# Performance work log

Measured on AMD Instinct MI355X. Metric: run time of the kernel, lower is better.

## Reference

```python
import jax, jax.numpy as jnp
import numpy as np

BETA = 0.25


def setup_inputs() -> dict:
    key = jax.random.key(0)
    k1, k2 = jax.random.split(key)
    x = jax.random.normal(k1, (32, 64, 64, 64), dtype=jnp.float32)   # [B, C, H, W]
    emb = jax.random.normal(k2, (1024, 64), dtype=jnp.float32)       # [K, C] codebook
    return {"x": x, "emb": emb}


def reference(x, emb):
    b, c, h, w = x.shape
    # (b h w) c
    z = jnp.transpose(x, (0, 2, 3, 1)).reshape(-1, c)
    # squared euclidean distances (argmin identical to torch.cdist argmin)
    # ||z||^2 - 2 z e^T + ||e||^2, never taking sqrt since only argmin is used
    d = (jnp.sum(z * z, axis=1, keepdims=True)
         - 2.0 * jnp.einsum('nc,kc->nk', z, emb)
         + jnp.sum(emb * emb, axis=1)[None, :])        # [N, K]
    idx = jnp.argmin(d, axis=1)                        # [N] int
    e = emb[idx]                                       # gather [N, C]
    e = jnp.transpose(e.reshape(b, h, w, c), (0, 3, 1, 2))  # [B, C, H, W]
    codebook_loss = jnp.mean((jax.lax.stop_gradient(x) - e) ** 2)
    commitment_loss = BETA * jnp.mean((x - jax.lax.stop_gradient(e)) ** 2)
    loss = codebook_loss + commitment_loss
    o = x + jax.lax.stop_gradient(e - x)               # straight-through
    indices = idx.reshape(b, h, w)
    return (o, loss, indices)
```

## Files before the change

kernel.cpp:

```cpp
#include <hip/hip_runtime.h>

#define BATCH   32
#define CCH     64
#define HW      4096
#define NPIX    (BATCH * HW)
#define KCODES  1024
#define NELEM   (NPIX * CCH)
#define MB      256
#define CK      64
#define MARGIN_Q 3u

typedef _Float16 f16;
typedef __attribute__((ext_vector_type(8))) _Float16 f16x8;
typedef __attribute__((ext_vector_type(4))) float    f32x4;

static __device__ __forceinline__ f32x4 mfma16(f16x8 a, f16x8 b, f32x4 c) {
    return __builtin_amdgcn_mfma_f32_16x16x32_f16(a, b, c, 0, 0, 0);
}

static __device__ __forceinline__ void dma16(void* lds, const void* g) {
    __builtin_amdgcn_global_load_lds(
        (const __attribute__((address_space(1))) unsigned int*)g,
        (__attribute__((address_space(3))) unsigned int*)lds, 16, 0, 0);
}

#define WS_EEB_F   64
#define WS_CBH_B   8192
#define WS_CBL_B   139264
#define WS_WL_U    67584

__global__ __launch_bounds__(256) void vq_prep(
    const float* __restrict__ emb, float* __restrict__ wsf,
    unsigned* __restrict__ wsu, f16* __restrict__ cbH, f16* __restrict__ cbL,
    float* __restrict__ eeb_g)
{
    const int t = threadIdx.x;
    if (blockIdx.x < 32) {
        const int gid = blockIdx.x * 256 + t;
        const int row = gid >> 3, gi = gid & 7;
        const float* src = emb + (size_t)row * CCH + gi * 8;
        float4 v0 = *(const float4*)(src);
        float4 v1 = *(const float4*)(src + 4);
        float vv[8] = {v0.x, v0.y, v0.z, v0.w, v1.x, v1.y, v1.z, v1.w};
        f16x8 h, l;
#pragma unroll
        for (int j = 0; j < 8; ++j) {
            f16 hh = (f16)vv[j];
            h[j] = hh;
            l[j] = (f16)(vv[j] - (float)hh);
        }
        const int off = row * 64 + 8 * (gi ^ (row & 7));
        *(f16x8*)(cbH + off) = h;
        *(f16x8*)(cbL + off) = l;
    } else {
        if (t == 0) { wsf[0] = 0.f; wsu[1] = 0u; }
        for (int r = t * 4; r < t * 4 + 4; ++r) {
            const float4* row4 = (const float4*)(emb + (size_t)r * CCH);
            float s = 0.f;
#pragma unroll
            for (int i = 0; i < 16; ++i) {
                float4 v = row4[i];
                s = fmaf(v.x, v.x, s); s = fmaf(v.y, v.y, s);
                s = fmaf(v.z, v.z, s); s = fmaf(v.w, v.w, s);
            }
            eeb_g[r] = fmaf(s, 2048.0f, 1048576.0f);
        }
    }
}

__global__ __launch_bounds__(256, 2) void vq_main(
    const float* __restrict__ x,
    const float* __restrict__ emb,
    const f16* __restrict__ cbH, const f16* __restrict__ cbL,
    const float* __restrict__ eeb_g,
    float* __restrict__ o, float* __restrict__ idx_out,
    float* __restrict__ acc, unsigned* __restrict__ wl_count,
    unsigned* __restrict__ wl, unsigned cap)
{
    __shared__ __align__(16) char smem[32768];
    __shared__ float eebl[2][CK];
    __shared__ unsigned bu1[MB], bu2[MB];
    __shared__ float wred[4];

    const int t    = threadIdx.x;
    const int lane = t & 63;
    const int w    = t >> 6;
    const int col  = lane & 15;
    const int quad = lane >> 4;
    const int c7   = col & 7;
    const int sw0  = 8 * (quad ^ c7);
    const int sw1  = sw0 ^ 32;
    const int n0   = blockIdx.x * MB;
    const int b    = n0 >> 12;
    const int p0   = n0 & 4095;
    const float* xb = x + (size_t)b * (CCH * HW) + p0;

    auto stage = [&](int chunk, int bufi) {
        const int k0 = chunk * CK;
        char* lb = smem + bufi * 16384;
        const char* gH = (const char*)cbH + (size_t)k0 * 128 + w * 2048 + lane * 16;
        const char* gL = (const char*)cbL + (size_t)k0 * 128 + w * 2048 + lane * 16;
        char* lH = lb + w * 2048;
        char* lL = lb + 8192 + w * 2048;
        dma16(lH,        gH);
        dma16(lH + 1024, gH + 1024);
        dma16(lL,        gL);
        dma16(lL + 1024, gL + 1024);
        if (t < CK) eebl[bufi][t] = eeb_g[k0 + t];
    };

    stage(0, 0);

    f16x8 aH[4][2], aL[4][2];
#pragma unroll
    for (int rt = 0; rt < 4; ++rt) {
        const int pp = w * 64 + rt * 16 + col;
#pragma unroll
        for (int kc = 0; kc < 2; ++kc) {
            f16x8 h, l;
#pragma unroll
            for (int j = 0; j < 8; ++j) {
                const int c = kc * 32 + quad * 8 + j;
                float zs = -2.0f * xb[(size_t)c * HW + pp];
                f16 hh = (f16)zs;
                h[j] = hh;
                l[j] = (f16)(zs - (float)hh);
            }
            aH[rt][kc] = h;
            aL[rt][kc] = l;
        }
    }

    unsigned best[16], best2[16];
#pragma unroll
    for (int s = 0; s < 16; ++s) { best[s] = 0xFFFFFFFFu; best2[s] = 0xFFFFFFFFu; }

    for (int chunk = 0; chunk < KCODES / CK; ++chunk) {
        const int cur = chunk & 1;
        __syncthreads();
        if (chunk + 1 < KCODES / CK) stage(chunk + 1, cur ^ 1);

        const f16* bufH = (const f16*)(smem + cur * 16384);
        const f16* bufL = bufH + 4096;
        const int k0 = chunk * CK;

#pragma unroll
        for (int tile = 0; tile < CK / 16; ++tile) {
            const f16* bh = bufH + (tile * 16 + col) * 64;
            const f16* bl = bufL + (tile * 16 + col) * 64;
            f16x8 bH0 = *(const f16x8*)(bh + sw0);
            f16x8 bH1 = *(const f16x8*)(bh + sw1);
            f16x8 bL0 = *(const f16x8*)(bl + sw0);
            f16x8 bL1 = *(const f16x8*)(bl + sw1);
            const float eebc = eebl[cur][tile * 16 + col];
            const unsigned kb = (unsigned)(k0 + tile * 16 + col);
#pragma unroll
            for (int rt = 0; rt < 4; ++rt) {
                f32x4 a4 = {0.f, 0.f, 0.f, 0.f};
                a4 = mfma16(aH[rt][0], bH0, a4);
                a4 = mfma16(aH[rt][1], bH1, a4);
                a4 = mfma16(aL[rt][0], bH0, a4);
                a4 = mfma16(aL[rt][1], bH1, a4);
                a4 = mfma16(aH[rt][0], bL0, a4);
                a4 = mfma16(aH[rt][1], bL1, a4);
#pragma unroll
                for (int r = 0; r < 4; ++r) {
                    float uf = fmaf(a4[r], 2048.0f, eebc);
                    unsigned pk = (((unsigned)uf) << 10) | kb;
                    const int s = rt * 4 + r;
                    best2[s] = min(best2[s], max(pk, best[s]));
                    best[s]  = min(best[s], pk);
                }
            }
        }
    }

#pragma unroll
    for (int d = 1; d < 16; d <<= 1) {
#pragma unroll
        for (int s = 0; s < 16; ++s) {
            unsigned ob  = __shfl_xor(best[s],  d, 64);
            unsigned ob2 = __shfl_xor(best2[s], d, 64);
            best2[s] = min(min(best2[s], ob2), max(best[s], ob));
            best[s]  = min(best[s], ob);
        }
    }
    if (col == 0) {
#pragma unroll
        for (int rt = 0; rt < 4; ++rt)
#pragma unroll
            for (int r = 0; r < 4; ++r) {
                const int pl = w * 64 + rt * 16 + quad * 4 + r;
                bu1[pl] = best[rt * 4 + r];
                bu2[pl] = best2[rt * 4 + r];
            }
    }
    __syncthreads();

    const unsigned bu = bu1[t];
    const unsigned bidx = bu & 1023u;
    idx_out[n0 + t] = (float)bidx;
    {
        const unsigned qg = (bu2[t] >> 10) - (bu >> 10);
        if (qg < MARGIN_Q) {
            unsigned pos = atomicAdd(wl_count, 1u);
            if (pos < cap) wl[pos] = (unsigned)(n0 + t);
        }
    }
    float ss = 0.f;
    {
        const float4* er4 = (const float4*)(emb + (size_t)bidx * CCH);
        const float* xbt = xb + t;
        float* ob = o + (size_t)b * (CCH * HW) + p0 + t;
#pragma unroll
        for (int i = 0; i < 16; ++i) {
            float4 ev = er4[i];
            float evv[4] = {ev.x, ev.y, ev.z, ev.w};
#pragma unroll
            for (int q = 0; q < 4; ++q) {
                const int c = i * 4 + q;
                float xv = xbt[(size_t)c * HW];
                float e  = evv[q];
                ob[(size_t)c * HW] = xv + (e - xv);
                float d = xv - e;
                ss = fmaf(d, d, ss);
            }
        }
    }
    for (int off = 32; off; off >>= 1) ss += __shfl_down(ss, off, 64);
    if (lane == 0) wred[w] = ss;
    __syncthreads();
    if (t == 0) atomicAdd(acc, (wred[0] + wred[1]) + (wred[2] + wred[3]));
}

__global__ __launch_bounds__(256) void vq_refine(
    const float* __restrict__ x, const float* __restrict__ emb,
    float* __restrict__ o, float* __restrict__ idx_out,
    float* __restrict__ acc, const unsigned* __restrict__ wl_count,
    const unsigned* __restrict__ wl, unsigned cap)
{
    __shared__ float zsh[CCH];
    __shared__ double rbd[4];
    __shared__ int rbi[4];
    __shared__ int s_pk;
    unsigned cnt = *wl_count; if (cnt > cap) cnt = cap;
    const int t = threadIdx.x;

    for (unsigned i = blockIdx.x; i < cnt; i += gridDim.x) {
        const int n = (int)wl[i];
        const int b = n >> 12, p = n & 4095;
        if (t < CCH) zsh[t] = x[(size_t)b * (CCH * HW) + (size_t)t * HW + p];
        __syncthreads();

        double bd = 1e300; int bi = KCODES;
        for (int j = 0; j < 4; ++j) {
            const int k = t + j * 256;
            const float* er = emb + (size_t)k * CCH;
            double d = 0.0;
#pragma unroll
            for (int c = 0; c < CCH; ++c) {
                double tt = (double)zsh[c] - (double)er[c];
                d = fma(tt, tt, d);
            }
            if (d < bd) { bd = d; bi = k; }
        }
        for (int dlt = 1; dlt < 64; dlt <<= 1) {
            double od = __shfl_xor(bd, dlt, 64);
            int    oi = __shfl_xor(bi, dlt, 64);
            if (od < bd || (od == bd && oi < bi)) { bd = od; bi = oi; }
        }
        const int wv = t >> 6;
        if ((t & 63) == 0) { rbd[wv] = bd; rbi[wv] = bi; }
        __syncthreads();
        if (t == 0) {
            double fb = rbd[0]; int fi = rbi[0];
            for (int q = 1; q < 4; ++q)
                if (rbd[q] < fb || (rbd[q] == fb && rbi[q] < fi)) { fb = rbd[q]; fi = rbi[q]; }
            const int old = (int)idx_out[n];
            if (fi != old) { idx_out[n] = (float)fi; s_pk = (old << 16) | fi; }
            else s_pk = -1;
        }
        __syncthreads();
        const int pk = s_pk;
        if (pk >= 0 && t < CCH) {
            const int old = pk >> 16, fi = pk & 0xFFFF;
            const float xv = zsh[t];
            const float eo = emb[(size_t)old * CCH + t];
            const float en = emb[(size_t)fi  * CCH + t];
            o[(size_t)b * (CCH * HW) + (size_t)t * HW + p] = xv + (en - xv);
            const float dn = xv - en, dd = xv - eo;
            float delta = dn * dn - dd * dd;
            for (int off = 32; off; off >>= 1) delta += __shfl_down(delta, off, 64);
            if (t == 0) atomicAdd(acc, delta);
        }
        __syncthreads();
    }
}

__global__ void vq_fin(const float* __restrict__ acc, float* __restrict__ loss) {
    *loss = 1.25f * (*acc) * (1.0f / (float)NELEM);
}

extern "C" void kernel_launch(void* const* d_in, const int* in_sizes, int n_in,
                              void* d_out, int out_size, void* d_ws, size_t ws_size,
                              hipStream_t stream) {
    const float* x   = (const float*)d_in[0];
    const float* emb = (const float*)d_in[1];
    float*    out = (float*)d_out;
    float*    wsf = (float*)d_ws;
    unsigned* wsu = (unsigned*)d_ws;
    char*     wsb = (char*)d_ws;

    float* o_out    = out;
    float* loss_out = out + NELEM;
    float* idx_out  = out + NELEM + 1;
    float* eeb_g    = wsf + WS_EEB_F;
    f16*   cbH      = (f16*)(wsb + WS_CBH_B);
    f16*   cbL      = (f16*)(wsb + WS_CBL_B);
    unsigned* wl    = wsu + WS_WL_U;
    unsigned cap = 0;
    if (ws_size / 4 > WS_WL_U) {
        size_t c = ws_size / 4 - WS_WL_U;
        cap = (unsigned)(c > NPIX ? NPIX : c);
    }

    vq_prep<<<33, 256, 0, stream>>>(emb, wsf, wsu, cbH, cbL, eeb_g);
    vq_main<<<NPIX / MB, 256, 0, stream>>>(x, emb, cbH, cbL, eeb_g, o_out,
                                           idx_out, wsf, wsu + 1, wl, cap);
    vq_refine<<<512, 256, 0, stream>>>(x, emb, o_out, idx_out, wsf,
                                       wsu + 1, wl, cap);
    vq_fin<<<1, 1, 0, stream>>>(wsf, loss_out);
}
```

Before: 159.3 us.

## Split codebook search across two blocks per pixel tile and merge in post kernel

The main distance kernel now splits the 1024-code search into two halves handled by separate blocks, doubling the grid and raising the occupancy hint. Per-half best and second-best packed keys go to workspace, and a new post kernel merges them, writes indices and output, accumulates the loss and builds the refine worklist. The refine margin is tightened, its grid doubled, and its fp64 distance loop split into four accumulators for ILP. This trades more parallelism for an extra kernel launch, extra global traffic for the partial results, and a reload of x in the post kernel.

```diff
diff --git a/kernel.cpp b/kernel.cpp
--- a/kernel.cpp
+++ b/kernel.cpp
@@ -8,7 +8,8 @@
 #define NELEM   (NPIX * CCH)
 #define MB      256
 #define CK      64
-#define MARGIN_Q 3u
+#define KSPLIT  2
+#define MARGIN_Q 2u
 
 typedef _Float16 f16;
 typedef __attribute__((ext_vector_type(8))) _Float16 f16x8;
@@ -27,7 +28,9 @@
 #define WS_EEB_F   64
 #define WS_CBH_B   8192
 #define WS_CBL_B   139264
-#define WS_WL_U    67584
+#define WS_PB1_U   67584
+#define WS_PB2_U   329728
+#define WS_WL_U    591872
 
 __global__ __launch_bounds__(256) void vq_prep(
     const float* __restrict__ emb, float* __restrict__ wsf,
@@ -68,19 +71,15 @@
     }
 }
 
-__global__ __launch_bounds__(256, 2) void vq_main(
+__global__ __launch_bounds__(256, 4) void vq_main(
     const float* __restrict__ x,
-    const float* __restrict__ emb,
     const f16* __restrict__ cbH, const f16* __restrict__ cbL,
     const float* __restrict__ eeb_g,
-    float* __restrict__ o, float* __restrict__ idx_out,
-    float* __restrict__ acc, unsigned* __restrict__ wl_count,
-    unsigned* __restrict__ wl, unsigned cap)
+    unsigned* __restrict__ pb1, unsigned* __restrict__ pb2)
 {
     __shared__ __align__(16) char smem[32768];
     __shared__ float eebl[2][CK];
     __shared__ unsigned bu1[MB], bu2[MB];
-    __shared__ float wred[4];
 
     const int t    = threadIdx.x;
     const int lane = t & 63;
@@ -90,13 +89,16 @@
     const int c7   = col & 7;
     const int sw0  = 8 * (quad ^ c7);
     const int sw1  = sw0 ^ 32;
-    const int n0   = blockIdx.x * MB;
+    const int half = blockIdx.x & 1;
+    const int gb   = blockIdx.x >> 1;
+    const int n0   = gb * MB;
     const int b    = n0 >> 12;
     const int p0   = n0 & 4095;
+    const int ch0  = half * (KCODES / CK / KSPLIT);
     const float* xb = x + (size_t)b * (CCH * HW) + p0;
 
-    auto stage = [&](int chunk, int bufi) {
-        const int k0 = chunk * CK;
+    auto stage = [&](int chunkAbs, int bufi) {
+        const int k0 = chunkAbs * CK;
         char* lb = smem + bufi * 16384;
         const char* gH = (const char*)cbH + (size_t)k0 * 128 + w * 2048 + lane * 16;
         const char* gL = (const char*)cbL + (size_t)k0 * 128 + w * 2048 + lane * 16;
@@ -109,7 +111,7 @@
         if (t < CK) eebl[bufi][t] = eeb_g[k0 + t];
     };
 
-    stage(0, 0);
+    stage(ch0, 0);
 
     f16x8 aH[4][2], aL[4][2];
 #pragma unroll
@@ -135,14 +137,15 @@
 #pragma unroll
     for (int s = 0; s < 16; ++s) { best[s] = 0xFFFFFFFFu; best2[s] = 0xFFFFFFFFu; }
 
-    for (int chunk = 0; chunk < KCODES / CK; ++chunk) {
+    const int NCH = KCODES / CK / KSPLIT;
+    for (int chunk = 0; chunk < NCH; ++chunk) {
         const int cur = chunk & 1;
         __syncthreads();
-        if (chunk + 1 < KCODES / CK) stage(chunk + 1, cur ^ 1);
+        if (chunk + 1 < NCH) stage(ch0 + chunk + 1, cur ^ 1);
 
         const f16* bufH = (const f16*)(smem + cur * 16384);
         const f16* bufL = bufH + 4096;
-        const int k0 = chunk * CK;
+        const int k0 = (ch0 + chunk) * CK;
 
 #pragma unroll
         for (int tile = 0; tile < CK / 16; ++tile) {
@@ -197,21 +200,40 @@
     }
     __syncthreads();
 
-    const unsigned bu = bu1[t];
+    pb1[half * NPIX + n0 + t] = bu1[t];
+    pb2[half * NPIX + n0 + t] = bu2[t];
+}
+
+__global__ __launch_bounds__(256) void vq_post(
+    const float* __restrict__ x, const float* __restrict__ emb,
+    const unsigned* __restrict__ pb1, const unsigned* __restrict__ pb2,
+    float* __restrict__ o, float* __restrict__ idx_out,
+    float* __restrict__ acc, unsigned* __restrict__ wl_count,
+    unsigned* __restrict__ wl, unsigned cap)
+{
+    __shared__ float wred[4];
+    const int t = threadIdx.x;
+    const int lane = t & 63, w = t >> 6;
+    const int n = blockIdx.x * 256 + t;
+    const int b = n >> 12, p = n & 4095;
+
+    const unsigned b0 = pb1[n], b1 = pb1[NPIX + n];
+    const unsigned s0 = pb2[n], s1 = pb2[NPIX + n];
+    const unsigned bu  = min(b0, b1);
+    const unsigned bu2 = min(min(s0, s1), max(b0, b1));
     const unsigned bidx = bu & 1023u;
-    idx_out[n0 + t] = (float)bidx;
-    {
-        const unsigned qg = (bu2[t] >> 10) - (bu >> 10);
-        if (qg < MARGIN_Q) {
-            unsigned pos = atomicAdd(wl_count, 1u);
-            if (pos < cap) wl[pos] = (unsigned)(n0 + t);
-        }
-    }
+    idx_out[n] = (float)bidx;
+    const unsigned qg = (bu2 >> 10) - (bu >> 10);
+    if (qg < MARGIN_Q) {
+        unsigned pos = atomicAdd(wl_count, 1u);
+        if (pos < cap) wl[pos] = (unsigned)n;
+    }
+
     float ss = 0.f;
     {
         const float4* er4 = (const float4*)(emb + (size_t)bidx * CCH);
-        const float* xbt = xb + t;
-        float* ob = o + (size_t)b * (CCH * HW) + p0 + t;
+        const float* xbt = x + (size_t)b * (CCH * HW) + p;
+        float* ob = o + (size_t)b * (CCH * HW) + p;
 #pragma unroll
         for (int i = 0; i < 16; ++i) {
             float4 ev = er4[i];
@@ -256,12 +278,17 @@
         for (int j = 0; j < 4; ++j) {
             const int k = t + j * 256;
             const float* er = emb + (size_t)k * CCH;
-            double d = 0.0;
-#pragma unroll
-            for (int c = 0; c < CCH; ++c) {
-                double tt = (double)zsh[c] - (double)er[c];
-                d = fma(tt, tt, d);
-            }
+            double d0 = 0.0, d1 = 0.0, d2 = 0.0, d3 = 0.0;
+#pragma unroll
+            for (int c = 0; c < CCH; c += 4) {
+                double t0 = (double)zsh[c + 0] - (double)er[c + 0];
+                double t1 = (double)zsh[c + 1] - (double)er[c + 1];
+                double t2 = (double)zsh[c + 2] - (double)er[c + 2];
+                double t3 = (double)zsh[c + 3] - (double)er[c + 3];
+                d0 = fma(t0, t0, d0); d1 = fma(t1, t1, d1);
+                d2 = fma(t2, t2, d2); d3 = fma(t3, t3, d3);
+            }
+            double d = (d0 + d1) + (d2 + d3);
             if (d < bd) { bd = d; bi = k; }
         }
         for (int dlt = 1; dlt < 64; dlt <<= 1) {
@@ -317,6 +344,8 @@
     float* eeb_g    = wsf + WS_EEB_F;
     f16*   cbH      = (f16*)(wsb + WS_CBH_B);
     f16*   cbL      = (f16*)(wsb + WS_CBL_B);
+    unsigned* pb1   = wsu + WS_PB1_U;
+    unsigned* pb2   = wsu + WS_PB2_U;
     unsigned* wl    = wsu + WS_WL_U;
     unsigned cap = 0;
     if (ws_size / 4 > WS_WL_U) {
@@ -325,9 +354,10 @@
     }
 
     vq_prep<<<33, 256, 0, stream>>>(emb, wsf, wsu, cbH, cbL, eeb_g);
-    vq_main<<<NPIX / MB, 256, 0, stream>>>(x, emb, cbH, cbL, eeb_g, o_out,
-                                           idx_out, wsf, wsu + 1, wl, cap);
-    vq_refine<<<512, 256, 0, stream>>>(x, emb, o_out, idx_out, wsf,
-                                       wsu + 1, wl, cap);
+    vq_main<<<(NPIX / MB) * KSPLIT, 256, 0, stream>>>(x, cbH, cbL, eeb_g, pb1, pb2);
+    vq_post<<<NPIX / 256, 256, 0, stream>>>(x, emb, pb1, pb2, o_out, idx_out,
+                                            wsf, wsu + 1, wl, cap);
+    vq_refine<<<1024, 256, 0, stream>>>(x, emb, o_out, idx_out, wsf,
+                                        wsu + 1, wl, cap);
     vq_fin<<<1, 1, 0, stream>>>(wsf, loss_out);
 }
```

Measured after the change: 315.2 us. +97.9%, slower.
